# Kernel tuning notes

Hardware: AMD Instinct MI355X
Metric: run time of the kernel (lower is better)

## Reference

```python
import jax, jax.numpy as jnp
import numpy as np

C = 256
CQ = C // 4


def setup_inputs() -> dict:
    key = jax.random.key(0)
    ks = jax.random.split(key, 7)
    B, H, W = 4, 64, 64
    x = jax.random.normal(ks[0], (B, C, H, W), dtype=jnp.float32)
    s = 1.0 / np.sqrt(C)
    Wq = jax.random.normal(ks[1], (CQ, C), dtype=jnp.float32) * s
    bq = jnp.zeros((CQ,), dtype=jnp.float32)
    Wk = jax.random.normal(ks[2], (CQ, C), dtype=jnp.float32) * s
    bk = jnp.zeros((CQ,), dtype=jnp.float32)
    Wv = jax.random.normal(ks[3], (C, C), dtype=jnp.float32) * s
    bv = jnp.zeros((C,), dtype=jnp.float32)
    gamma = jnp.zeros((1,), dtype=jnp.float32)
    return {"x": x, "Wq": Wq, "bq": bq, "Wk": Wk, "bk": bk,
            "Wv": Wv, "bv": bv, "gamma": gamma}


def reference(x, Wq, bq, Wk, bk, Wv, bv, gamma):
    B, Cc, Hh, Ww = x.shape
    N = Hh * Ww
    xf = x.reshape(B, Cc, N)                      # [B, C, N]
    # 1x1 convs are channel-mixing matmuls
    q = jnp.einsum('oc,bcn->bon', Wq, xf) + bq[None, :, None]   # [B, C/4, N]
    k = jnp.einsum('oc,bcn->bon', Wk, xf) + bk[None, :, None]   # [B, C/4, N]
    v = jnp.einsum('oc,bcn->bon', Wv, xf) + bv[None, :, None]   # [B, C, N]
    energy = jnp.einsum('bci,bcj->bij', q, k)     # [B, N, N] (unscaled)
    attn = jax.nn.softmax(energy, axis=-1)
    out = jnp.einsum('bcj,bij->bci', v, attn)     # [B, C, N]
    out = out.reshape(B, Cc, Hh, Ww)
    return gamma[0] * out + x
```

## Files before the change

kernel.cpp:

```cpp
#include <hip/hip_runtime.h>
#include <hip/hip_bf16.h>

typedef unsigned short u16;
typedef unsigned int u32;
typedef float f32x4 __attribute__((ext_vector_type(4)));
typedef short s16x8 __attribute__((ext_vector_type(8)));

#define MFMA16(a, b, c) __builtin_amdgcn_mfma_f32_16x16x32_bf16(a, b, c, 0, 0, 0)

#define NN 4096
#define CC 256
#define CQ 64

__device__ __forceinline__ u16 f2bf(float x) {
    union { float f; u32 u; } v; v.f = x;
    return (u16)((v.u + 0x7FFFu + ((v.u >> 16) & 1u)) >> 16);
}
__device__ __forceinline__ float bf2f(u16 u) {
    union { u32 u; float f; } v; v.u = ((u32)u) << 16;
    return v.f;
}
__device__ __forceinline__ void gll16(const void* g, void* l) {
    __builtin_amdgcn_global_load_lds(
        (const __attribute__((address_space(1))) void*)g,
        (__attribute__((address_space(3))) void*)l, 16, 0, 0);
}

__global__ __launch_bounds__(256) void prep(
    const float* __restrict__ x, const float* __restrict__ Wq,
    const float* __restrict__ Wk, const float* __restrict__ Wv,
    u16* __restrict__ xT, u16* __restrict__ wbf)
{
    const int bid = blockIdx.x, t = threadIdx.x;
    if (bid < 1024) {
        __shared__ float tile[64 * 65];
        const int b = bid >> 8, ctile = (bid >> 6) & 3, ntile = bid & 63;
        const int c0 = ctile * 64, n0 = ntile * 64;
        const int cw = t >> 4, nj = (t & 15) * 4;
        for (int it = 0; it < 4; it++) {
            const int ci = it * 16 + cw;
            const float4 v4 = *(const float4*)(x + ((size_t)(b * CC + c0 + ci)) * NN + n0 + nj);
            tile[(nj + 0) * 65 + ci] = v4.x;
            tile[(nj + 1) * 65 + ci] = v4.y;
            tile[(nj + 2) * 65 + ci] = v4.z;
            tile[(nj + 3) * 65 + ci] = v4.w;
        }
        __syncthreads();
        const int r = t >> 2, c16 = (t & 3) * 16;
        union { u16 h[16]; uint4 q[2]; } pk;
        for (int j = 0; j < 16; j++) pk.h[j] = f2bf(tile[r * 65 + c16 + j]);
        u16* dst = xT + ((size_t)(b * NN + n0 + r)) * CC + c0 + c16;
        *(uint4*)dst = pk.q[0];
        *(uint4*)(dst + 8) = pk.q[1];
    } else {
        const int flat = (bid - 1024) * 1024 + t * 4;
        const int o = flat >> 8, c = flat & 255;
        const float* src = (o < 64)  ? (Wq + (size_t)o * CC + c)
                         : (o < 128) ? (Wk + (size_t)(o - 64) * CC + c)
                                     : (Wv + (size_t)(o - 128) * CC + c);
        const float4 v4 = *(const float4*)src;
        union { u16 h[4]; uint2 d; } pk;
        pk.h[0] = f2bf(v4.x); pk.h[1] = f2bf(v4.y);
        pk.h[2] = f2bf(v4.z); pk.h[3] = f2bf(v4.w);
        *(uint2*)(wbf + (size_t)o * CC + c) = pk.d;
    }
}

__global__ __launch_bounds__(512, 4) void qkv(
    const u16* __restrict__ xT, const u16* __restrict__ wbf,
    const float* __restrict__ bq, const float* __restrict__ bk,
    const float* __restrict__ bv,
    u16* __restrict__ qT, u16* __restrict__ kT, u16* __restrict__ v)
{
    __shared__ __align__(16) u16 sm[384 * 64 + 32 * 64];
    u16* Ws = sm;
    u16* Xs = sm + 384 * 64;

    const int bid = blockIdx.x;
    const int b = bid >> 7, n0 = (bid & 127) * 32;
    const int t = threadIdx.x, lane = t & 63, w = t >> 6;
    const int col = lane & 15, quad = lane >> 4;

    f32x4 acc[3][2];
    for (int i = 0; i < 3; i++) { acc[i][0] = f32x4{0,0,0,0}; acc[i][1] = f32x4{0,0,0,0}; }

    for (int cc = 0; cc < 4; cc++) {
        const int c0 = cc * 64;
        for (int m = 0; m < 6; m++) {
            const int g = m * 512 + t;
            const int row = g >> 3, ch = g & 7;
            gll16(wbf + (size_t)row * CC + c0 + ((ch ^ (row & 7)) * 8), Ws + g * 8);
        }
        if (w < 4) {
            const int g = w * 64 + lane;
            const int n = g >> 3, ch = g & 7;
            gll16(xT + ((size_t)(b * NN + n0 + n)) * CC + c0 + ((ch ^ (n & 7)) * 8),
                  Xs + g * 8);
        }
        __syncthreads();
        for (int kk = 0; kk < 2; kk++) {
            s16x8 bx[2];
            for (int nt2 = 0; nt2 < 2; nt2++) {
                const int n = nt2 * 16 + col;
                bx[nt2] = *(const s16x8*)&Xs[n * 64 + (((kk * 4 + quad) ^ (n & 7)) * 8)];
            }
            for (int ot = 0; ot < 3; ot++) {
                const int row = w * 48 + ot * 16 + col;
                const s16x8 a = *(const s16x8*)&Ws[row * 64 + (((kk * 4 + quad) ^ (row & 7)) * 8)];
                acc[ot][0] = MFMA16(a, bx[0], acc[ot][0]);
                acc[ot][1] = MFMA16(a, bx[1], acc[ot][1]);
            }
        }
        __syncthreads();
    }
    for (int ot = 0; ot < 3; ot++) {
        const int og = w * 48 + ot * 16 + quad * 4;
        for (int nt2 = 0; nt2 < 2; nt2++) {
            const int n = n0 + nt2 * 16 + col;
            if (og < 64) {
                union { u16 h[4]; uint2 d; } pk;
                for (int r = 0; r < 4; r++) pk.h[r] = f2bf(acc[ot][nt2][r] + bq[og + r]);
                *(uint2*)(qT + ((size_t)(b * NN + n)) * CQ + og) = pk.d;
            } else if (og < 128) {
                union { u16 h[4]; uint2 d; } pk;
                for (int r = 0; r < 4; r++) pk.h[r] = f2bf(acc[ot][nt2][r] + bk[og - 64 + r]);
                *(uint2*)(kT + ((size_t)(b * NN + n)) * CQ + (og - 64)) = pk.d;
            } else {
                for (int r = 0; r < 4; r++)
                    v[((size_t)(b * CC + og - 128 + r)) * NN + n] =
                        f2bf(acc[ot][nt2][r] + bv[og - 128 + r]);
            }
        }
    }
}

__global__ __launch_bounds__(512, 4) void flash_attn(
    const u16* __restrict__ qT, const u16* __restrict__ kT,
    const u16* __restrict__ v,
    u16* __restrict__ Op0, float* __restrict__ Op1,
    float* __restrict__ lws)
{
    __shared__ __align__(16) u16 sm[24576];
    __shared__ float ls[2][64];

    const int bid = blockIdx.x;
    const int p = bid & 7;
    const int b = p >> 1, jh = p & 1;
    const int n0 = (bid >> 3) * 64;
    const int jb = jh * 2048;
    const int t = threadIdx.x;
    const int lane = t & 63, wv = t >> 6;
    const int col = lane & 15, quad = lane >> 4;
    const int strip = wv & 3, jhi = wv >> 2;
    const int ih = wv >> 2, cq = wv & 3;

    const int swz8 = (quad ^ ((col >> 1) & 3)) * 8;

    s16x8 aq[2];
    {
        const u16* qp = qT + ((size_t)(b * NN + n0 + strip * 16 + col)) * CQ + quad * 8;
        aq[0] = *(const s16x8*)qp;
        aq[1] = *(const s16x8*)(qp + 32);
    }

    f32x4 o_[2][4];
    for (int i = 0; i < 2; i++) for (int j = 0; j < 4; j++) o_[i][j] = f32x4{0,0,0,0};
    float lac[4] = {0.f, 0.f, 0.f, 0.f};

    const int kg = wv * 64 + lane;
    const int krow = kg >> 3;
    const u16* ksrc = kT + ((size_t)(b * NN + jb + krow)) * CQ + (((kg & 7) ^ (krow & 7)) * 8);
    const int kdo = kg * 8;
    const u16* vsrc[2];
    int vdo[2];
    for (int m = 0; m < 2; m++) {
        const int g = m * 512 + t;
        const int row = g >> 2;
        vdo[m] = g * 8;
        vsrc[m] = v + ((size_t)(b * CC + row)) * NN + jb
                    + (((g & 3) ^ ((row >> 1) & 3)) * 8);
    }

    auto issueK = [&](int jt, int kb) {
        if (wv < 4) gll16(ksrc + (size_t)jt * 32 * CQ, sm + kb * 2048 + kdo);
    };
    auto issueV = [&](int jt, int vb) {
        u16* base = sm + 4096 + vb * 8192;
        for (int m = 0; m < 2; m++)
            gll16(vsrc[m] + jt * 32, base + vdo[m]);
    };
    auto S_phase = [&](int kb, int pb) {
        const u16* Kb = sm + kb * 2048;
        u16* Pb = sm + 20480 + pb * 2048;
        f32x4 s = f32x4{0,0,0,0};
        for (int kk = 0; kk < 2; kk++) {
            const int jrow = jhi * 16 + col;
            const s16x8 bk_ = *(const s16x8*)
                &Kb[jrow * 64 + (((kk * 4 + quad) ^ (jrow & 7)) * 8)];
            s = MFMA16(aq[kk], bk_, s);
        }
        const int jch = jhi * 2 + (col >> 3);
        const int jin = col & 7;
        for (int r = 0; r < 4; r++) {
            const float pv = __expf(fminf(s[r], 60.f));
            lac[r] += pv;
            const int rrow = strip * 16 + quad * 4 + r;
            Pb[rrow * 32 + ((jch ^ ((quad * 2 + (r >> 1)) & 3)) * 8) + jin] = f2bf(pv);
        }
    };
    auto PV_phase = [&](int pb, int vb) {
        const u16* Pb = sm + 20480 + pb * 2048;
        const u16* Vb = sm + 4096 + vb * 8192;
        s16x8 pa[2];
        for (int it2 = 0; it2 < 2; it2++)
            pa[it2] = *(const s16x8*)&Pb[((ih * 2 + it2) * 16 + col) * 32 + swz8];
        for (int ct = 0; ct < 4; ct++) {
            const int c = cq * 64 + ct * 16 + col;
            const s16x8 bv_ = *(const s16x8*)&Vb[c * 32 + swz8];
            o_[0][ct] = MFMA16(pa[0], bv_, o_[0][ct]);
            o_[1][ct] = MFMA16(pa[1], bv_, o_[1][ct]);
        }
    };

    issueK(0, 0);
    issueV(0, 0);
    issueK(1, 1);
    __syncthreads();
    S_phase(0, 0);

    int vcur = 0, pcur = 0;
    for (int m = 0; m < 64; m++) {
        __syncthreads();
        issueV((m + 1 < 64) ? m + 1 : 63, vcur ^ 1);
        issueK((m + 2 < 64) ? m + 2 : 63, m & 1);
        PV_phase(pcur, vcur);
        if (m < 63) S_phase((m + 1) & 1, pcur ^ 1);
        vcur ^= 1; pcur ^= 1;
    }

    for (int r = 0; r < 4; r++) {
        float lv = lac[r];
        lv += __shfl_xor(lv, 1, 64);
        lv += __shfl_xor(lv, 2, 64);
        lv += __shfl_xor(lv, 4, 64);
        lv += __shfl_xor(lv, 8, 64);
        lac[r] = lv;
    }
    if (col == 0)
        for (int r = 0; r < 4; r++)
            ls[jhi][strip * 16 + quad * 4 + r] = lac[r];
    __syncthreads();
    if (t < 64)
        lws[(size_t)jh * 4 * NN + (size_t)b * NN + n0 + t] = ls[0][t] + ls[1][t];

    float* Tf = (float*)sm;
    u16*  Tu = sm;
    for (int rd = 0; rd < 2; rd++) {
        if ((cq >> 1) == rd) {
            const int cl = (cq & 1) * 64;
            for (int it2 = 0; it2 < 2; it2++) {
                const int ib = (ih * 2 + it2) * 16 + quad * 4;
                for (int ct = 0; ct < 4; ct++) {
                    const int c = cl + ct * 16 + col;
                    if (jh == 0) {
                        union { u16 h[4]; uint2 d; } pk;
                        for (int r = 0; r < 4; r++) pk.h[r] = f2bf(o_[it2][ct][r]);
                        *(uint2*)&Tu[c * 136 + ib] = pk.d;
                    } else {
                        *(float2*)&Tf[c * 68 + ib] = float2{o_[it2][ct][0], o_[it2][ct][1]};
                        *(float2*)&Tf[c * 68 + ib + 2] = float2{o_[it2][ct][2], o_[it2][ct][3]};
                    }
                }
            }
        }
        __syncthreads();
        const int cl = t >> 2, i0 = (t & 3) * 16;
        const int c = rd * 128 + cl;
        if (jh == 0) {
            u16* dst = Op0 + ((size_t)(b * CC + c)) * NN + n0 + i0;
            *(uint4*)dst       = *(const uint4*)&Tu[cl * 136 + i0];
            *(uint4*)(dst + 8) = *(const uint4*)&Tu[cl * 136 + i0 + 8];
        } else {
            float* dst = Op1 + ((size_t)(b * CC + c)) * NN + n0 + i0;
            for (int k = 0; k < 4; k++)
                *(float4*)(dst + k * 4) = *(const float4*)&Tf[cl * 68 + i0 + k * 4];
        }
        __syncthreads();
    }
}

__global__ __launch_bounds__(256) void combine(
    const float* __restrict__ x, const u16* __restrict__ Op0,
    const float* __restrict__ lws, const float* __restrict__ gamma,
    float* __restrict__ out)
{
    const size_t idx = ((size_t)blockIdx.x * 256 + threadIdx.x) * 4;
    const int b = (int)(idx >> 20);
    const int n = (int)(idx & (NN - 1));
    const float g = gamma[0];
    const float4 xv = *(const float4*)(x + idx);
    const float4 o1 = *(const float4*)(out + idx);
    union { uint2 d; u16 h[4]; } o0;
    o0.d = *(const uint2*)(Op0 + idx);
    const float4 l0 = *(const float4*)(lws + (size_t)b * NN + n);
    const float4 l1 = *(const float4*)(lws + (size_t)4 * NN + (size_t)b * NN + n);
    float4 r;
    r.x = xv.x + g * (bf2f(o0.h[0]) + o1.x) / (l0.x + l1.x);
    r.y = xv.y + g * (bf2f(o0.h[1]) + o1.y) / (l0.y + l1.y);
    r.z = xv.z + g * (bf2f(o0.h[2]) + o1.z) / (l0.z + l1.z);
    r.w = xv.w + g * (bf2f(o0.h[3]) + o1.w) / (l0.w + l1.w);
    *(float4*)(out + idx) = r;
}

extern "C" void kernel_launch(void* const* d_in, const int* in_sizes, int n_in,
                              void* d_out, int out_size, void* d_ws, size_t ws_size,
                              hipStream_t stream)
{
    const float* x     = (const float*)d_in[0];
    const float* Wq    = (const float*)d_in[1];
    const float* bq    = (const float*)d_in[2];
    const float* Wk    = (const float*)d_in[3];
    const float* bk    = (const float*)d_in[4];
    const float* Wv    = (const float*)d_in[5];
    const float* bv    = (const float*)d_in[6];
    const float* gamma = (const float*)d_in[7];
    float* out = (float*)d_out;

    u16* xT  = (u16*)d_ws;
    u16* wbf = xT  + (size_t)4 * NN * CC;
    u16* qTw = wbf + (size_t)384 * CC;
    u16* kTw = qTw + (size_t)4 * NN * CQ;
    u16* vw  = kTw + (size_t)4 * NN * CQ;
    u16* Op0 = xT;
    float* lws = (float*)wbf;

    prep<<<1120, 256, 0, stream>>>(x, Wq, Wk, Wv, xT, wbf);
    qkv<<<512, 512, 0, stream>>>(xT, wbf, bq, bk, bv, qTw, kTw, vw);
    flash_attn<<<512, 512, 0, stream>>>(qTw, kTw, vw, Op0, out, lws);
    combine<<<4096, 256, 0, stream>>>(x, Op0, lws, gamma, out);
}
```

Measured before the change: 167.4 us.

## Give each wave private P tiles and merge S/PV into one phase per tile

```diff
diff --git a/kernel.cpp b/kernel.cpp
--- a/kernel.cpp
+++ b/kernel.cpp
@@ -141,7 +141,7 @@
     float* __restrict__ lws)
 {
     __shared__ __align__(16) u16 sm[24576];
-    __shared__ float ls[2][64];
+    __shared__ float ls[64];
 
     const int bid = blockIdx.x;
     const int p = bid & 7;
@@ -151,21 +151,21 @@
     const int t = threadIdx.x;
     const int lane = t & 63, wv = t >> 6;
     const int col = lane & 15, quad = lane >> 4;
-    const int strip = wv & 3, jhi = wv >> 2;
-    const int ih = wv >> 2, cq = wv & 3;
+    const int qt = wv & 3, ch = wv >> 2;
 
     const int swz8 = (quad ^ ((col >> 1) & 3)) * 8;
-
-    s16x8 aq[2];
+    const int cx = col & 3;
+
+    s16x8 qfrag[2];
     {
-        const u16* qp = qT + ((size_t)(b * NN + n0 + strip * 16 + col)) * CQ + quad * 8;
-        aq[0] = *(const s16x8*)qp;
-        aq[1] = *(const s16x8*)(qp + 32);
-    }
-
-    f32x4 o_[2][4];
-    for (int i = 0; i < 2; i++) for (int j = 0; j < 4; j++) o_[i][j] = f32x4{0,0,0,0};
-    float lac[4] = {0.f, 0.f, 0.f, 0.f};
+        const u16* qp = qT + ((size_t)(b * NN + n0 + qt * 16 + col)) * CQ + quad * 8;
+        qfrag[0] = *(const s16x8*)qp;
+        qfrag[1] = *(const s16x8*)(qp + 32);
+    }
+
+    f32x4 o_[8];
+    for (int j = 0; j < 8; j++) o_[j] = f32x4{0,0,0,0};
+    float lac = 0.f;
 
     const int kg = wv * 64 + lane;
     const int krow = kg >> 3;
@@ -189,87 +189,71 @@
         for (int m = 0; m < 2; m++)
             gll16(vsrc[m] + jt * 32, base + vdo[m]);
     };
-    auto S_phase = [&](int kb, int pb) {
-        const u16* Kb = sm + kb * 2048;
-        u16* Pb = sm + 20480 + pb * 2048;
-        f32x4 s = f32x4{0,0,0,0};
-        for (int kk = 0; kk < 2; kk++) {
-            const int jrow = jhi * 16 + col;
-            const s16x8 bk_ = *(const s16x8*)
-                &Kb[jrow * 64 + (((kk * 4 + quad) ^ (jrow & 7)) * 8)];
-            s = MFMA16(aq[kk], bk_, s);
-        }
-        const int jch = jhi * 2 + (col >> 3);
-        const int jin = col & 7;
+
+    u16* Pw = sm + 20480 + wv * 512;
+
+    auto compute = [&](int m) {
+        const u16* Kb = sm + (m & 1) * 2048;
+        const u16* Vb = sm + 4096 + (m & 1) * 8192;
+        f32x4 sa0 = f32x4{0,0,0,0}, sa1 = f32x4{0,0,0,0};
+        for (int ckh = 0; ckh < 2; ckh++) {
+            const int kc = (((ckh * 4 + quad) ^ (col & 7)) * 8);
+            const s16x8 k0 = *(const s16x8*)&Kb[col * 64 + kc];
+            const s16x8 k1 = *(const s16x8*)&Kb[(16 + col) * 64 + kc];
+            sa0 = MFMA16(k0, qfrag[ckh], sa0);
+            sa1 = MFMA16(k1, qfrag[ckh], sa1);
+        }
+        float p0[4], p1[4];
         for (int r = 0; r < 4; r++) {
-            const float pv = __expf(fminf(s[r], 60.f));
-            lac[r] += pv;
-            const int rrow = strip * 16 + quad * 4 + r;
-            Pb[rrow * 32 + ((jch ^ ((quad * 2 + (r >> 1)) & 3)) * 8) + jin] = f2bf(pv);
-        }
-    };
-    auto PV_phase = [&](int pb, int vb) {
-        const u16* Pb = sm + 20480 + pb * 2048;
-        const u16* Vb = sm + 4096 + vb * 8192;
-        s16x8 pa[2];
-        for (int it2 = 0; it2 < 2; it2++)
-            pa[it2] = *(const s16x8*)&Pb[((ih * 2 + it2) * 16 + col) * 32 + swz8];
-        for (int ct = 0; ct < 4; ct++) {
-            const int c = cq * 64 + ct * 16 + col;
+            p0[r] = __expf(fminf(sa0[r], 60.f));
+            p1[r] = __expf(fminf(sa1[r], 60.f));
+            lac += p0[r] + p1[r];
+        }
+        u32* Pr = (u32*)&Pw[col * 32];
+        const int q2 = (quad & 1) << 1;
+        Pr[((((quad >> 1)    ) ^ cx) << 2) + q2 + 0] = (u32)f2bf(p0[0]) | ((u32)f2bf(p0[1]) << 16);
+        Pr[((((quad >> 1)    ) ^ cx) << 2) + q2 + 1] = (u32)f2bf(p0[2]) | ((u32)f2bf(p0[3]) << 16);
+        Pr[(((2 + (quad >> 1)) ^ cx) << 2) + q2 + 0] = (u32)f2bf(p1[0]) | ((u32)f2bf(p1[1]) << 16);
+        Pr[(((2 + (quad >> 1)) ^ cx) << 2) + q2 + 1] = (u32)f2bf(p1[2]) | ((u32)f2bf(p1[3]) << 16);
+        const s16x8 pa = *(const s16x8*)&Pw[col * 32 + ((quad ^ cx) * 8)];
+        #pragma unroll
+        for (int ct = 0; ct < 8; ct++) {
+            const int c = ch * 128 + ct * 16 + col;
             const s16x8 bv_ = *(const s16x8*)&Vb[c * 32 + swz8];
-            o_[0][ct] = MFMA16(pa[0], bv_, o_[0][ct]);
-            o_[1][ct] = MFMA16(pa[1], bv_, o_[1][ct]);
+            o_[ct] = MFMA16(pa, bv_, o_[ct]);
         }
     };
 
     issueK(0, 0);
     issueV(0, 0);
-    issueK(1, 1);
+    for (int m = 0; m < 64; m++) {
+        __syncthreads();
+        const int jn = (m + 1 < 64) ? m + 1 : 63;
+        issueK(jn, (m + 1) & 1);
+        issueV(jn, (m + 1) & 1);
+        compute(m);
+    }
+
+    lac += __shfl_xor(lac, 16, 64);
+    lac += __shfl_xor(lac, 32, 64);
+    if (ch == 0 && lane < 16) ls[qt * 16 + lane] = lac;
     __syncthreads();
-    S_phase(0, 0);
-
-    int vcur = 0, pcur = 0;
-    for (int m = 0; m < 64; m++) {
-        __syncthreads();
-        issueV((m + 1 < 64) ? m + 1 : 63, vcur ^ 1);
-        issueK((m + 2 < 64) ? m + 2 : 63, m & 1);
-        PV_phase(pcur, vcur);
-        if (m < 63) S_phase((m + 1) & 1, pcur ^ 1);
-        vcur ^= 1; pcur ^= 1;
-    }
-
-    for (int r = 0; r < 4; r++) {
-        float lv = lac[r];
-        lv += __shfl_xor(lv, 1, 64);
-        lv += __shfl_xor(lv, 2, 64);
-        lv += __shfl_xor(lv, 4, 64);
-        lv += __shfl_xor(lv, 8, 64);
-        lac[r] = lv;
-    }
-    if (col == 0)
-        for (int r = 0; r < 4; r++)
-            ls[jhi][strip * 16 + quad * 4 + r] = lac[r];
-    __syncthreads();
-    if (t < 64)
-        lws[(size_t)jh * 4 * NN + (size_t)b * NN + n0 + t] = ls[0][t] + ls[1][t];
+    if (t < 64) lws[(size_t)jh * 4 * NN + (size_t)b * NN + n0 + t] = ls[t];
 
     float* Tf = (float*)sm;
     u16*  Tu = sm;
     for (int rd = 0; rd < 2; rd++) {
-        if ((cq >> 1) == rd) {
-            const int cl = (cq & 1) * 64;
-            for (int it2 = 0; it2 < 2; it2++) {
-                const int ib = (ih * 2 + it2) * 16 + quad * 4;
-                for (int ct = 0; ct < 4; ct++) {
-                    const int c = cl + ct * 16 + col;
-                    if (jh == 0) {
-                        union { u16 h[4]; uint2 d; } pk;
-                        for (int r = 0; r < 4; r++) pk.h[r] = f2bf(o_[it2][ct][r]);
-                        *(uint2*)&Tu[c * 136 + ib] = pk.d;
-                    } else {
-                        *(float2*)&Tf[c * 68 + ib] = float2{o_[it2][ct][0], o_[it2][ct][1]};
-                        *(float2*)&Tf[c * 68 + ib + 2] = float2{o_[it2][ct][2], o_[it2][ct][3]};
-                    }
+        if (ch == rd) {
+            const int ib = qt * 16 + quad * 4;
+            for (int ct = 0; ct < 8; ct++) {
+                const int cl = ct * 16 + col;
+                if (jh == 0) {
+                    union { u16 h[4]; uint2 d; } pk;
+                    for (int r = 0; r < 4; r++) pk.h[r] = f2bf(o_[ct][r]);
+                    *(uint2*)&Tu[cl * 136 + ib] = pk.d;
+                } else {
+                    *(float2*)&Tf[cl * 68 + ib]     = float2{o_[ct][0], o_[ct][1]};
+                    *(float2*)&Tf[cl * 68 + ib + 2] = float2{o_[ct][2], o_[ct][3]};
                 }
             }
         }
```

Result: slower. 184.6 us (+10.3%).

## Fuse bf16 conversion and transpose of x and weights into the qkv kernel

Applied to the files above, without the earlier changes.

```diff
diff --git a/kernel.cpp b/kernel.cpp
--- a/kernel.cpp
+++ b/kernel.cpp
@@ -26,76 +26,36 @@
         (__attribute__((address_space(3))) void*)l, 16, 0, 0);
 }
 
-__global__ __launch_bounds__(256) void prep(
-    const float* __restrict__ x, const float* __restrict__ Wq,
-    const float* __restrict__ Wk, const float* __restrict__ Wv,
-    u16* __restrict__ xT, u16* __restrict__ wbf)
-{
-    const int bid = blockIdx.x, t = threadIdx.x;
-    if (bid < 1024) {
-        __shared__ float tile[64 * 65];
-        const int b = bid >> 8, ctile = (bid >> 6) & 3, ntile = bid & 63;
-        const int c0 = ctile * 64, n0 = ntile * 64;
-        const int cw = t >> 4, nj = (t & 15) * 4;
-        for (int it = 0; it < 4; it++) {
-            const int ci = it * 16 + cw;
-            const float4 v4 = *(const float4*)(x + ((size_t)(b * CC + c0 + ci)) * NN + n0 + nj);
-            tile[(nj + 0) * 65 + ci] = v4.x;
-            tile[(nj + 1) * 65 + ci] = v4.y;
-            tile[(nj + 2) * 65 + ci] = v4.z;
-            tile[(nj + 3) * 65 + ci] = v4.w;
-        }
-        __syncthreads();
-        const int r = t >> 2, c16 = (t & 3) * 16;
-        union { u16 h[16]; uint4 q[2]; } pk;
-        for (int j = 0; j < 16; j++) pk.h[j] = f2bf(tile[r * 65 + c16 + j]);
-        u16* dst = xT + ((size_t)(b * NN + n0 + r)) * CC + c0 + c16;
-        *(uint4*)dst = pk.q[0];
-        *(uint4*)(dst + 8) = pk.q[1];
-    } else {
-        const int flat = (bid - 1024) * 1024 + t * 4;
-        const int o = flat >> 8, c = flat & 255;
-        const float* src = (o < 64)  ? (Wq + (size_t)o * CC + c)
-                         : (o < 128) ? (Wk + (size_t)(o - 64) * CC + c)
-                                     : (Wv + (size_t)(o - 128) * CC + c);
-        const float4 v4 = *(const float4*)src;
-        union { u16 h[4]; uint2 d; } pk;
-        pk.h[0] = f2bf(v4.x); pk.h[1] = f2bf(v4.y);
-        pk.h[2] = f2bf(v4.z); pk.h[3] = f2bf(v4.w);
-        *(uint2*)(wbf + (size_t)o * CC + c) = pk.d;
-    }
-}
-
 __global__ __launch_bounds__(512, 4) void qkv(
-    const u16* __restrict__ xT, const u16* __restrict__ wbf,
+    const float* __restrict__ x,
+    const float* __restrict__ Wq, const float* __restrict__ Wk,
+    const float* __restrict__ Wv,
     const float* __restrict__ bq, const float* __restrict__ bk,
     const float* __restrict__ bv,
     u16* __restrict__ qT, u16* __restrict__ kT, u16* __restrict__ v)
 {
-    __shared__ __align__(16) u16 sm[384 * 64 + 32 * 64];
-    u16* Ws = sm;
-    u16* Xs = sm + 384 * 64;
+    __shared__ __align__(16) u16 Xs[32 * 64];
 
     const int bid = blockIdx.x;
     const int b = bid >> 7, n0 = (bid & 127) * 32;
     const int t = threadIdx.x, lane = t & 63, w = t >> 6;
     const int col = lane & 15, quad = lane >> 4;
+    const int xrow = t >> 3, xseg = t & 7;
 
     f32x4 acc[3][2];
     for (int i = 0; i < 3; i++) { acc[i][0] = f32x4{0,0,0,0}; acc[i][1] = f32x4{0,0,0,0}; }
 
     for (int cc = 0; cc < 4; cc++) {
         const int c0 = cc * 64;
-        for (int m = 0; m < 6; m++) {
-            const int g = m * 512 + t;
-            const int row = g >> 3, ch = g & 7;
-            gll16(wbf + (size_t)row * CC + c0 + ((ch ^ (row & 7)) * 8), Ws + g * 8);
-        }
-        if (w < 4) {
-            const int g = w * 64 + lane;
-            const int n = g >> 3, ch = g & 7;
-            gll16(xT + ((size_t)(b * NN + n0 + n)) * CC + c0 + ((ch ^ (n & 7)) * 8),
-                  Xs + g * 8);
+        const float4 xv = *(const float4*)(
+            x + ((size_t)(b * CC + c0 + xrow)) * NN + n0 + xseg * 4);
+        __syncthreads();
+        {
+            const float xe[4] = {xv.x, xv.y, xv.z, xv.w};
+            for (int i = 0; i < 4; i++) {
+                const int n = xseg * 4 + i;
+                Xs[n * 64 + (((xrow >> 3) ^ (n & 7)) * 8) + (xrow & 7)] = f2bf(xe[i]);
+            }
         }
         __syncthreads();
         for (int kk = 0; kk < 2; kk++) {
@@ -106,12 +66,20 @@
             }
             for (int ot = 0; ot < 3; ot++) {
                 const int row = w * 48 + ot * 16 + col;
-                const s16x8 a = *(const s16x8*)&Ws[row * 64 + (((kk * 4 + quad) ^ (row & 7)) * 8)];
-                acc[ot][0] = MFMA16(a, bx[0], acc[ot][0]);
-                acc[ot][1] = MFMA16(a, bx[1], acc[ot][1]);
-            }
-        }
-        __syncthreads();
+                const float* wsrc = (row < 64)  ? (Wq + (size_t)row * CC)
+                                  : (row < 128) ? (Wk + (size_t)(row - 64) * CC)
+                                                : (Wv + (size_t)(row - 128) * CC);
+                const float4 a0 = *(const float4*)(wsrc + c0 + kk * 32 + quad * 8);
+                const float4 a1 = *(const float4*)(wsrc + c0 + kk * 32 + quad * 8 + 4);
+                union { u16 h[8]; s16x8 v8; } ap;
+                ap.h[0] = f2bf(a0.x); ap.h[1] = f2bf(a0.y);
+                ap.h[2] = f2bf(a0.z); ap.h[3] = f2bf(a0.w);
+                ap.h[4] = f2bf(a1.x); ap.h[5] = f2bf(a1.y);
+                ap.h[6] = f2bf(a1.z); ap.h[7] = f2bf(a1.w);
+                acc[ot][0] = MFMA16(ap.v8, bx[0], acc[ot][0]);
+                acc[ot][1] = MFMA16(ap.v8, bx[1], acc[ot][1]);
+            }
+        }
     }
     for (int ot = 0; ot < 3; ot++) {
         const int og = w * 48 + ot * 16 + quad * 4;
@@ -326,16 +294,13 @@
     const float* gamma = (const float*)d_in[7];
     float* out = (float*)d_out;
 
-    u16* xT  = (u16*)d_ws;
-    u16* wbf = xT  + (size_t)4 * NN * CC;
-    u16* qTw = wbf + (size_t)384 * CC;
-    u16* kTw = qTw + (size_t)4 * NN * CQ;
-    u16* vw  = kTw + (size_t)4 * NN * CQ;
-    u16* Op0 = xT;
-    float* lws = (float*)wbf;
-
-    prep<<<1120, 256, 0, stream>>>(x, Wq, Wk, Wv, xT, wbf);
-    qkv<<<512, 512, 0, stream>>>(xT, wbf, bq, bk, bv, qTw, kTw, vw);
+    u16* Op0   = (u16*)d_ws;
+    float* lws = (float*)(Op0 + (size_t)4 * NN * CC);
+    u16* qTw   = (u16*)(lws + (size_t)8 * NN);
+    u16* kTw   = qTw + (size_t)4 * NN * CQ;
+    u16* vw    = kTw + (size_t)4 * NN * CQ;
+
+    qkv<<<512, 512, 0, stream>>>(x, Wq, Wk, Wv, bq, bk, bv, qTw, kTw, vw);
     flash_attn<<<512, 512, 0, stream>>>(qTw, kTw, vw, Op0, out, lws);
     combine<<<4096, 256, 0, stream>>>(x, Op0, lws, gamma, out);
 }
```

Result: slower. 179.2 us (+7.1%).
